# Kernel optimization log

Measured on AMD Instinct MI355X. Metric: run time of the kernel, lower is better.

Reference implementation:

```python
import jax, jax.numpy as jnp
import numpy as np

TEMPERATURE = 0.1
EPS = 1e-8


def setup_inputs() -> dict:
    key = jax.random.key(0)
    k1, k2 = jax.random.split(key)
    features = jax.random.normal(k1, (1024, 256, 16, 8), dtype=jnp.float32)
    labels = jax.random.randint(k2, (1024,), 0, 64, dtype=jnp.int64)
    return {"features": features, "labels": labels}


def reference(features, labels):
    B = features.shape[0]
    f = features.reshape(B, -1)
    norm = jnp.clip(jnp.linalg.norm(f, axis=1, keepdims=True), EPS)
    f = f / norm
    # matcher modeled as cosine-similarity gram matrix (opaque TransMatcher out of scope)
    scores = (f @ f.T) / TEMPERATURE  # [B, B]

    same = labels[:, None] == labels[None, :]
    eye = jnp.eye(B, dtype=bool)
    pos = same & ~eye  # positives excluding self
    neg = ~same & ~eye  # negatives excluding self

    # shared max over pos ∪ neg = all off-diagonal entries per row (matches original)
    row_max = jnp.max(jnp.where(eye, -jnp.inf, scores), axis=1, keepdims=True)
    e = jnp.exp(scores - row_max)  # [B, B]
    pos_sum = jnp.sum(jnp.where(pos, e, 0.0), axis=1)
    neg_sum = jnp.sum(jnp.where(neg, e, 0.0), axis=1)

    valid = jnp.any(pos, axis=1) & jnp.any(neg, axis=1)
    safe_pos = jnp.where(valid, pos_sum, 1.0)
    safe_neg = jnp.where(valid, neg_sum, 1.0)
    # loss_i = neg_term - pos_term; shared max cancels
    loss_i = jnp.where(valid, jnp.log(safe_neg) - jnp.log(safe_pos), 0.0)

    total = jnp.sum(valid.astype(jnp.float32))
    loss = jnp.where(total > 0, jnp.sum(loss_i) / jnp.maximum(total, 1.0), 0.0)

    max_pos = jnp.max(jnp.where(pos, scores, -jnp.inf), axis=1)
    max_neg = jnp.max(jnp.where(neg, scores, -jnp.inf), axis=1)
    correct = jnp.sum((valid & (max_pos > max_neg)).astype(jnp.float32))
    accuracy = jnp.where(total > 0, correct / jnp.maximum(total, 1.0), 0.5)
    return loss, accuracy
```

## Files before the change

kernel.cpp:

```cpp
#include <hip/hip_runtime.h>
#include <hip/hip_bf16.h>
#include <stdint.h>

#define BSZ 1024
#define KF 32768
#define SPLITK 32
#define KPER (KF / SPLITK)
#define BKB 128
#define TEMP_INV 10.0f

typedef float f32x4 __attribute__((ext_vector_type(4)));

__device__ __forceinline__ void async_copy16(const void* g, void* l) {
    __builtin_amdgcn_global_load_lds(
        (const __attribute__((address_space(1))) void*)g,
        (__attribute__((address_space(3))) void*)l, 16, 0, 0);
}

__device__ __forceinline__ unsigned short f2bf_bits(float x) {
    union { float f; uint32_t u; } t; t.f = x;
    uint32_t r = t.u + 0x7FFFu + ((t.u >> 16) & 1u);
    return (unsigned short)(r >> 16);
}
__device__ __forceinline__ float bf2f(unsigned short b) {
    union { uint32_t u; float f; } t; t.u = ((uint32_t)b) << 16; return t.f;
}

__device__ __forceinline__ float waveSum(float v) {
    for (int o = 32; o > 0; o >>= 1) v += __shfl_down(v, o);
    return v;
}
__device__ __forceinline__ float waveMax(float v) {
    for (int o = 32; o > 0; o >>= 1) v = fmaxf(v, __shfl_down(v, o));
    return v;
}
__device__ __forceinline__ float blockSum(float v, float* red, int tid) {
    v = waveSum(v);
    __syncthreads();
    if ((tid & 63) == 0) red[tid >> 6] = v;
    __syncthreads();
    return red[0] + red[1] + red[2] + red[3];
}
__device__ __forceinline__ float blockMax(float v, float* red, int tid) {
    v = waveMax(v);
    __syncthreads();
    if ((tid & 63) == 0) red[tid >> 6] = v;
    __syncthreads();
    return fmaxf(fmaxf(red[0], red[1]), fmaxf(red[2], red[3]));
}

__global__ __launch_bounds__(256) void k_norm_convert(
    const float* __restrict__ f, unsigned char* __restrict__ f8,
    float* __restrict__ inv_norm) {
    int row = blockIdx.x, tid = threadIdx.x;
    const float4* src = (const float4*)(f + (size_t)row * KF);
    int4* dst = (int4*)(f8 + (size_t)row * KF);
    float ss = 0.f;
    for (int o = 0; o < 8; ++o) {
        int base4 = o * 1024 + tid * 4;
        int4 pk;
        int* pkp = &pk.x;
#pragma unroll
        for (int q = 0; q < 4; ++q) {
            float4 v = src[base4 + q];
            ss += v.x * v.x + v.y * v.y + v.z * v.z + v.w * v.w;
            int wd = __builtin_amdgcn_cvt_pk_fp8_f32(v.x, v.y, 0, false);
            wd = __builtin_amdgcn_cvt_pk_fp8_f32(v.z, v.w, wd, true);
            pkp[q] = wd;
        }
        dst[o * 256 + tid] = pk;
    }
    __shared__ float red[4];
    float tot = blockSum(ss, red, tid);
    if (tid == 0) inv_norm[row] = 1.0f / fmaxf(sqrtf(tot), 1e-8f);
}

__global__ __launch_bounds__(256) void k_gemm(
    const unsigned char* __restrict__ f8, unsigned short* __restrict__ partials) {
    __shared__ unsigned char Alds[128 * BKB];
    __shared__ unsigned char Blds[128 * BKB];
    int tid = threadIdx.x;

    int t = blockIdx.x;
    int bi = 0, accu = 0;
    while (accu + bi + 1 <= t) { accu += bi + 1; ++bi; }
    int bj = t - accu;
    int row0 = bi * 128, col0 = bj * 128;
    int p = blockIdx.y;
    size_t kbase = (size_t)p * KPER;

    const unsigned char* Ag = f8 + (size_t)row0 * KF;
    const unsigned char* Bg = f8 + (size_t)col0 * KF;
    int lane = tid & 63, w = tid >> 6;
    int wrow = (w >> 1) * 64, wcol = (w & 1) * 64;
    int mrow = lane & 15, quad = lane >> 4;

    int r_st[4], g_st[4];
#pragma unroll
    for (int c = 0; c < 4; ++c) {
        int idx = c * 256 + tid;
        r_st[c] = idx >> 3;
        g_st[c] = (idx & 7) ^ (r_st[c] & 7);
    }

    f32x4 acc[4][4] = {};

    for (int kt = 0; kt < KPER / BKB; ++kt) {
        size_t k0 = kbase + (size_t)kt * BKB;
        __syncthreads();
#pragma unroll
        for (int c = 0; c < 4; ++c) {
            int idx = c * 256 + tid;
            async_copy16(Ag + (size_t)r_st[c] * KF + k0 + g_st[c] * 16, &Alds[idx * 16]);
            async_copy16(Bg + (size_t)r_st[c] * KF + k0 + g_st[c] * 16, &Blds[idx * 16]);
        }
        __syncthreads();
#pragma unroll
        for (int ks = 0; ks < 4; ++ks) {
            long av[4], bv[4];
            int chunk = ks * 2 + (quad >> 1);
            int sub = (quad & 1) * 8;
#pragma unroll
            for (int mi = 0; mi < 4; ++mi) {
                int row = wrow + mi * 16 + mrow;
                av[mi] = *(const long*)&Alds[row * BKB + (chunk ^ (row & 7)) * 16 + sub];
            }
#pragma unroll
            for (int ni = 0; ni < 4; ++ni) {
                int row = wcol + ni * 16 + mrow;
                bv[ni] = *(const long*)&Blds[row * BKB + (chunk ^ (row & 7)) * 16 + sub];
            }
#pragma unroll
            for (int mi = 0; mi < 4; ++mi)
#pragma unroll
                for (int ni = 0; ni < 4; ++ni)
                    acc[mi][ni] = __builtin_amdgcn_mfma_f32_16x16x32_fp8_fp8(
                        av[mi], bv[ni], acc[mi][ni], 0, 0, 0);
        }
    }

    unsigned short* outp = partials + (size_t)p * BSZ * BSZ;
#pragma unroll
    for (int mi = 0; mi < 4; ++mi)
#pragma unroll
        for (int ni = 0; ni < 4; ++ni)
#pragma unroll
            for (int r = 0; r < 4; ++r) {
                int row = row0 + wrow + mi * 16 + quad * 4 + r;
                int col = col0 + wcol + ni * 16 + mrow;
                outp[(size_t)row * BSZ + col] = f2bf_bits(acc[mi][ni][r]);
            }
    if (bi != bj) {
#pragma unroll
        for (int mi = 0; mi < 4; ++mi)
#pragma unroll
            for (int ni = 0; ni < 4; ++ni) {
                int rowm = col0 + wcol + ni * 16 + mrow;
                int colm = row0 + wrow + mi * 16 + quad * 4;
                ushort4 v;
                v.x = f2bf_bits(acc[mi][ni][0]);
                v.y = f2bf_bits(acc[mi][ni][1]);
                v.z = f2bf_bits(acc[mi][ni][2]);
                v.w = f2bf_bits(acc[mi][ni][3]);
                *(ushort4*)&outp[(size_t)rowm * BSZ + colm] = v;
            }
    }
}

__global__ __launch_bounds__(256) void k_loss_rows(
    const unsigned short* __restrict__ partials, const float* __restrict__ inv_norm,
    const int* __restrict__ labels, float* __restrict__ rloss,
    float* __restrict__ rvalid, float* __restrict__ rcorr) {
    int i = blockIdx.x, tid = threadIdx.x;
    __shared__ float srow[BSZ];
    __shared__ int slab[BSZ];
    __shared__ float red[4];
    for (int c = 0; c < 4; ++c) slab[c * 256 + tid] = labels[c * 256 + tid];
    float inv_i = inv_norm[i];

    int j4 = tid * 4;
    float sx = 0.f, sy = 0.f, sz = 0.f, sw = 0.f;
#pragma unroll
    for (int p2 = 0; p2 < SPLITK; ++p2) {
        ushort4 v = *(const ushort4*)&partials[(size_t)p2 * BSZ * BSZ + (size_t)i * BSZ + j4];
        sx += bf2f(v.x); sy += bf2f(v.y); sz += bf2f(v.z); sw += bf2f(v.w);
    }
    float4 invj = *(const float4*)&inv_norm[j4];
    srow[j4 + 0] = sx * inv_i * invj.x * TEMP_INV;
    srow[j4 + 1] = sy * inv_i * invj.y * TEMP_INV;
    srow[j4 + 2] = sz * inv_i * invj.z * TEMP_INV;
    srow[j4 + 3] = sw * inv_i * invj.w * TEMP_INV;
    __syncthreads();

    int lab_i = slab[i];
    float lm = -3.0e38f;
    for (int c = 0; c < 4; ++c) {
        int j = c * 256 + tid;
        if (j != i) lm = fmaxf(lm, srow[j]);
    }
    float rowmax = blockMax(lm, red, tid);

    float pos_sum = 0.f, neg_sum = 0.f, mp = -3.0e38f, mn = -3.0e38f;
    for (int c = 0; c < 4; ++c) {
        int j = c * 256 + tid;
        if (j == i) continue;
        float s = srow[j];
        float e = expf(s - rowmax);
        if (slab[j] == lab_i) { pos_sum += e; mp = fmaxf(mp, s); }
        else                  { neg_sum += e; mn = fmaxf(mn, s); }
    }
    float ps = blockSum(pos_sum, red, tid);
    float ns = blockSum(neg_sum, red, tid);
    float mpa = blockMax(mp, red, tid);
    float mna = blockMax(mn, red, tid);
    if (tid == 0) {
        bool valid = (mpa > -1.0e37f) && (mna > -1.0e37f);
        rloss[i]  = valid ? (logf(ns) - logf(ps)) : 0.f;
        rvalid[i] = valid ? 1.f : 0.f;
        rcorr[i]  = (valid && (mpa > mna)) ? 1.f : 0.f;
    }
}

__global__ __launch_bounds__(256) void k_final(
    const float* __restrict__ rloss, const float* __restrict__ rvalid,
    const float* __restrict__ rcorr, float* __restrict__ out) {
    __shared__ float red[4];
    int tid = threadIdx.x;
    float sl = 0.f, sv = 0.f, sc = 0.f;
    for (int c = 0; c < 4; ++c) {
        int j = c * 256 + tid;
        sl += rloss[j]; sv += rvalid[j]; sc += rcorr[j];
    }
    sl = blockSum(sl, red, tid);
    sv = blockSum(sv, red, tid);
    sc = blockSum(sc, red, tid);
    if (tid == 0) {
        out[0] = (sv > 0.f) ? sl / fmaxf(sv, 1.f) : 0.f;
        out[1] = (sv > 0.f) ? sc / fmaxf(sv, 1.f) : 0.5f;
    }
}

extern "C" void kernel_launch(void* const* d_in, const int* in_sizes, int n_in,
                              void* d_out, int out_size, void* d_ws, size_t ws_size,
                              hipStream_t stream) {
    const float* feats = (const float*)d_in[0];
    const int* labels = (const int*)d_in[1];
    float* out = (float*)d_out;
    char* ws = (char*)d_ws;

    unsigned char* f8        = (unsigned char*)ws;
    unsigned short* partials = (unsigned short*)(ws + (size_t)32 * 1024 * 1024);
    float* inv_norm          = (float*)(ws + (size_t)96 * 1024 * 1024);
    float* rloss             = inv_norm + BSZ;
    float* rvalid            = rloss + BSZ;
    float* rcorr             = rvalid + BSZ;

    k_norm_convert<<<BSZ, 256, 0, stream>>>(feats, f8, inv_norm);
    k_gemm<<<dim3(36, SPLITK), 256, 0, stream>>>(f8, partials);
    k_loss_rows<<<BSZ, 256, 0, stream>>>(partials, inv_norm, labels, rloss, rvalid, rcorr);
    k_final<<<1, 256, 0, stream>>>(rloss, rvalid, rcorr, out);
}
```

Before: 270.4 us.

## Use 16x16x128 scaled FP8 MFMA and load A operand directly from global

Replaces four 16x16x32 FP8 MFMAs per k-tile with a single 16x16x128 mfma_scale instruction using neutral scales (0x7F). A-operand tiles are loaded straight from global memory into registers instead of being staged through LDS, which halves the shared-memory footprint. Launch bounds now request 3 blocks per CU for occupancy. The direct global loads for A are not coalesced across the 128-row tile and are not prefetched, so they may add latency stalls.

```diff
diff --git a/kernel.cpp b/kernel.cpp
--- a/kernel.cpp
+++ b/kernel.cpp
@@ -10,6 +10,7 @@
 #define TEMP_INV 10.0f
 
 typedef float f32x4 __attribute__((ext_vector_type(4)));
+typedef int v8i __attribute__((ext_vector_type(8)));
 
 __device__ __forceinline__ void async_copy16(const void* g, void* l) {
     __builtin_amdgcn_global_load_lds(
@@ -75,9 +76,8 @@
     if (tid == 0) inv_norm[row] = 1.0f / fmaxf(sqrtf(tot), 1e-8f);
 }
 
-__global__ __launch_bounds__(256) void k_gemm(
+__global__ __launch_bounds__(256, 3) void k_gemm(
     const unsigned char* __restrict__ f8, unsigned short* __restrict__ partials) {
-    __shared__ unsigned char Alds[128 * BKB];
     __shared__ unsigned char Blds[128 * BKB];
     int tid = threadIdx.x;
 
@@ -103,40 +103,46 @@
         g_st[c] = (idx & 7) ^ (r_st[c] & 7);
     }
 
+    const int4* Arow[4];
+#pragma unroll
+    for (int mi = 0; mi < 4; ++mi)
+        Arow[mi] = (const int4*)(Ag + (size_t)(wrow + mi * 16 + mrow) * KF
+                                 + kbase + quad * 32);
+
     f32x4 acc[4][4] = {};
 
     for (int kt = 0; kt < KPER / BKB; ++kt) {
         size_t k0 = kbase + (size_t)kt * BKB;
         __syncthreads();
 #pragma unroll
-        for (int c = 0; c < 4; ++c) {
-            int idx = c * 256 + tid;
-            async_copy16(Ag + (size_t)r_st[c] * KF + k0 + g_st[c] * 16, &Alds[idx * 16]);
-            async_copy16(Bg + (size_t)r_st[c] * KF + k0 + g_st[c] * 16, &Blds[idx * 16]);
+        for (int c = 0; c < 4; ++c)
+            async_copy16(Bg + (size_t)r_st[c] * KF + k0 + g_st[c] * 16,
+                         &Blds[(c * 256 + tid) * 16]);
+        v8i a8[4];
+#pragma unroll
+        for (int mi = 0; mi < 4; ++mi) {
+            int4 lo = Arow[mi][kt * 8];
+            int4 hi = Arow[mi][kt * 8 + 1];
+            a8[mi] = (v8i){lo.x, lo.y, lo.z, lo.w, hi.x, hi.y, hi.z, hi.w};
         }
         __syncthreads();
-#pragma unroll
-        for (int ks = 0; ks < 4; ++ks) {
-            long av[4], bv[4];
-            int chunk = ks * 2 + (quad >> 1);
-            int sub = (quad & 1) * 8;
-#pragma unroll
-            for (int mi = 0; mi < 4; ++mi) {
-                int row = wrow + mi * 16 + mrow;
-                av[mi] = *(const long*)&Alds[row * BKB + (chunk ^ (row & 7)) * 16 + sub];
-            }
-#pragma unroll
-            for (int ni = 0; ni < 4; ++ni) {
-                int row = wcol + ni * 16 + mrow;
-                bv[ni] = *(const long*)&Blds[row * BKB + (chunk ^ (row & 7)) * 16 + sub];
-            }
-#pragma unroll
-            for (int mi = 0; mi < 4; ++mi)
-#pragma unroll
-                for (int ni = 0; ni < 4; ++ni)
-                    acc[mi][ni] = __builtin_amdgcn_mfma_f32_16x16x32_fp8_fp8(
-                        av[mi], bv[ni], acc[mi][ni], 0, 0, 0);
+        v8i b8[4];
+#pragma unroll
+        for (int ni = 0; ni < 4; ++ni) {
+            int rB = wcol + ni * 16 + mrow;
+            int4 lo = *(const int4*)&Blds[rB * BKB + ((quad * 2)     ^ (rB & 7)) * 16];
+            int4 hi = *(const int4*)&Blds[rB * BKB + ((quad * 2 + 1) ^ (rB & 7)) * 16];
+            b8[ni] = (v8i){lo.x, lo.y, lo.z, lo.w, hi.x, hi.y, hi.z, hi.w};
         }
+#pragma unroll
+        for (int mi = 0; mi < 4; ++mi)
+#pragma unroll
+            for (int ni = 0; ni < 4; ++ni)
+                acc[mi][ni] = __builtin_amdgcn_mfma_scale_f32_16x16x128_f8f6f4(
+                    a8[mi], b8[ni], acc[mi][ni],
+                    0, 0,
+                    0, 0x7F7F7F7F,
+                    0, 0x7F7F7F7F);
     }
 
     unsigned short* outp = partials + (size_t)p * BSZ * BSZ;
```

New measurement: 280.8 us. +3.9%, slower.

## Double-buffer B tiles, load A directly to registers, fuse final reduction

Applied to the files above, without the earlier changes.

The GEMM now loads A fragments straight from global memory into registers and stages only B through LDS. B is double-buffered with async global-to-LDS copies issued two iterations ahead, and explicit vmcnt waits plus raw barriers replace the two __syncthreads per k-step, so loads overlap with MFMA work. The A reads take 32 contiguous bytes per lane and the B reads use 16-byte LDS loads, which changes the k-ordering of fragments consistently for both operands. The final single-block kernel is removed: per-row results are accumulated with atomics and the last block, found by a ticket counter, writes the outputs. This adds the risk of hand-tuned waitcnt correctness and atomic ordering of the float sums.

```diff
diff --git a/kernel.cpp b/kernel.cpp
--- a/kernel.cpp
+++ b/kernel.cpp
@@ -7,6 +7,7 @@
 #define SPLITK 32
 #define KPER (KF / SPLITK)
 #define BKB 128
+#define NITER (KPER / BKB)
 #define TEMP_INV 10.0f
 
 typedef float f32x4 __attribute__((ext_vector_type(4)));
@@ -51,8 +52,9 @@
 
 __global__ __launch_bounds__(256) void k_norm_convert(
     const float* __restrict__ f, unsigned char* __restrict__ f8,
-    float* __restrict__ inv_norm) {
+    float* __restrict__ inv_norm, float* __restrict__ gaccum) {
     int row = blockIdx.x, tid = threadIdx.x;
+    if (row == 0 && tid < 4) gaccum[tid] = 0.f;
     const float4* src = (const float4*)(f + (size_t)row * KF);
     int4* dst = (int4*)(f8 + (size_t)row * KF);
     float ss = 0.f;
@@ -77,8 +79,7 @@
 
 __global__ __launch_bounds__(256) void k_gemm(
     const unsigned char* __restrict__ f8, unsigned short* __restrict__ partials) {
-    __shared__ unsigned char Alds[128 * BKB];
-    __shared__ unsigned char Blds[128 * BKB];
+    __shared__ unsigned char Blds[2][128 * BKB];
     int tid = threadIdx.x;
 
     int t = blockIdx.x;
@@ -102,41 +103,63 @@
         r_st[c] = idx >> 3;
         g_st[c] = (idx & 7) ^ (r_st[c] & 7);
     }
-
-    f32x4 acc[4][4] = {};
-
-    for (int kt = 0; kt < KPER / BKB; ++kt) {
-        size_t k0 = kbase + (size_t)kt * BKB;
-        __syncthreads();
+    auto stageB = [&](int buf, size_t koff) {
 #pragma unroll
         for (int c = 0; c < 4; ++c) {
             int idx = c * 256 + tid;
-            async_copy16(Ag + (size_t)r_st[c] * KF + k0 + g_st[c] * 16, &Alds[idx * 16]);
-            async_copy16(Bg + (size_t)r_st[c] * KF + k0 + g_st[c] * 16, &Blds[idx * 16]);
-        }
-        __syncthreads();
-#pragma unroll
-        for (int ks = 0; ks < 4; ++ks) {
-            long av[4], bv[4];
-            int chunk = ks * 2 + (quad >> 1);
-            int sub = (quad & 1) * 8;
-#pragma unroll
-            for (int mi = 0; mi < 4; ++mi) {
-                int row = wrow + mi * 16 + mrow;
-                av[mi] = *(const long*)&Alds[row * BKB + (chunk ^ (row & 7)) * 16 + sub];
-            }
-#pragma unroll
-            for (int ni = 0; ni < 4; ++ni) {
-                int row = wcol + ni * 16 + mrow;
-                bv[ni] = *(const long*)&Blds[row * BKB + (chunk ^ (row & 7)) * 16 + sub];
-            }
+            async_copy16(Bg + (size_t)r_st[c] * KF + koff + g_st[c] * 16,
+                         &Blds[buf][idx * 16]);
+        }
+    };
+
+    const unsigned char* Aptr[4];
+#pragma unroll
+    for (int mi = 0; mi < 4; ++mi)
+        Aptr[mi] = Ag + (size_t)(wrow + mi * 16 + mrow) * KF + kbase + quad * 32;
+
+    f32x4 acc[4][4] = {};
+    union I4L2 { int4 v; long l[2]; };
+
+    stageB(0, kbase);
+    stageB(1, kbase + BKB);
+
+#pragma unroll
+    for (int kt = 0; kt < NITER; ++kt) {
+        int cur = kt & 1;
+        long a_l[4][4];
+#pragma unroll
+        for (int mi = 0; mi < 4; ++mi) {
+            I4L2 u0, u1;
+            u0.v = *(const int4*)(Aptr[mi] + (size_t)kt * BKB);
+            u1.v = *(const int4*)(Aptr[mi] + (size_t)kt * BKB + 16);
+            a_l[mi][0] = u0.l[0]; a_l[mi][1] = u0.l[1];
+            a_l[mi][2] = u1.l[0]; a_l[mi][3] = u1.l[1];
+        }
+        if (kt < NITER - 1) asm volatile("s_waitcnt vmcnt(12)" ::: "memory");
+        else                asm volatile("s_waitcnt vmcnt(8)"  ::: "memory");
+        asm volatile("s_barrier" ::: "memory");
+
+        long b_l[4][4];
+#pragma unroll
+        for (int ni = 0; ni < 4; ++ni) {
+            int rB = wcol + ni * 16 + mrow;
+            I4L2 lo, hi;
+            lo.v = *(const int4*)&Blds[cur][rB * BKB + ((quad * 2)     ^ (rB & 7)) * 16];
+            hi.v = *(const int4*)&Blds[cur][rB * BKB + ((quad * 2 + 1) ^ (rB & 7)) * 16];
+            b_l[ni][0] = lo.l[0]; b_l[ni][1] = lo.l[1];
+            b_l[ni][2] = hi.l[0]; b_l[ni][3] = hi.l[1];
+        }
+#pragma unroll
+        for (int ts = 0; ts < 4; ++ts)
 #pragma unroll
             for (int mi = 0; mi < 4; ++mi)
 #pragma unroll
                 for (int ni = 0; ni < 4; ++ni)
                     acc[mi][ni] = __builtin_amdgcn_mfma_f32_16x16x32_fp8_fp8(
-                        av[mi], bv[ni], acc[mi][ni], 0, 0, 0);
-        }
+                        a_l[mi][ts], b_l[ni][ts], acc[mi][ni], 0, 0, 0);
+
+        asm volatile("s_barrier" ::: "memory");
+        if (kt + 2 < NITER) stageB(cur, kbase + (size_t)(kt + 2) * BKB);
     }
 
     unsigned short* outp = partials + (size_t)p * BSZ * BSZ;
@@ -169,12 +192,13 @@
 
 __global__ __launch_bounds__(256) void k_loss_rows(
     const unsigned short* __restrict__ partials, const float* __restrict__ inv_norm,
-    const int* __restrict__ labels, float* __restrict__ rloss,
-    float* __restrict__ rvalid, float* __restrict__ rcorr) {
+    const int* __restrict__ labels, float* __restrict__ gaccum,
+    float* __restrict__ out) {
     int i = blockIdx.x, tid = threadIdx.x;
     __shared__ float srow[BSZ];
     __shared__ int slab[BSZ];
     __shared__ float red[4];
+    __shared__ int s_ticket;
     for (int c = 0; c < 4; ++c) slab[c * 256 + tid] = labels[c * 256 + tid];
     float inv_i = inv_norm[i];
 
@@ -213,28 +237,21 @@
     float ns = blockSum(neg_sum, red, tid);
     float mpa = blockMax(mp, red, tid);
     float mna = blockMax(mn, red, tid);
+
     if (tid == 0) {
         bool valid = (mpa > -1.0e37f) && (mna > -1.0e37f);
-        rloss[i]  = valid ? (logf(ns) - logf(ps)) : 0.f;
-        rvalid[i] = valid ? 1.f : 0.f;
-        rcorr[i]  = (valid && (mpa > mna)) ? 1.f : 0.f;
-    }
-}
-
-__global__ __launch_bounds__(256) void k_final(
-    const float* __restrict__ rloss, const float* __restrict__ rvalid,
-    const float* __restrict__ rcorr, float* __restrict__ out) {
-    __shared__ float red[4];
-    int tid = threadIdx.x;
-    float sl = 0.f, sv = 0.f, sc = 0.f;
-    for (int c = 0; c < 4; ++c) {
-        int j = c * 256 + tid;
-        sl += rloss[j]; sv += rvalid[j]; sc += rcorr[j];
-    }
-    sl = blockSum(sl, red, tid);
-    sv = blockSum(sv, red, tid);
-    sc = blockSum(sc, red, tid);
-    if (tid == 0) {
+        float li = valid ? (logf(ns) - logf(ps)) : 0.f;
+        atomicAdd(&gaccum[0], li);
+        atomicAdd(&gaccum[1], valid ? 1.f : 0.f);
+        atomicAdd(&gaccum[2], (valid && (mpa > mna)) ? 1.f : 0.f);
+        __threadfence();
+        s_ticket = atomicAdd((int*)&gaccum[3], 1);
+    }
+    __syncthreads();
+    if (s_ticket == BSZ - 1 && tid == 0) {
+        float sl = atomicAdd(&gaccum[0], 0.f);
+        float sv = atomicAdd(&gaccum[1], 0.f);
+        float sc = atomicAdd(&gaccum[2], 0.f);
         out[0] = (sv > 0.f) ? sl / fmaxf(sv, 1.f) : 0.f;
         out[1] = (sv > 0.f) ? sc / fmaxf(sv, 1.f) : 0.5f;
     }
@@ -251,12 +268,9 @@
     unsigned char* f8        = (unsigned char*)ws;
     unsigned short* partials = (unsigned short*)(ws + (size_t)32 * 1024 * 1024);
     float* inv_norm          = (float*)(ws + (size_t)96 * 1024 * 1024);
-    float* rloss             = inv_norm + BSZ;
-    float* rvalid            = rloss + BSZ;
-    float* rcorr             = rvalid + BSZ;
-
-    k_norm_convert<<<BSZ, 256, 0, stream>>>(feats, f8, inv_norm);
+    float* gaccum            = inv_norm + BSZ;
+
+    k_norm_convert<<<BSZ, 256, 0, stream>>>(feats, f8, inv_norm, gaccum);
     k_gemm<<<dim3(36, SPLITK), 256, 0, stream>>>(f8, partials);
-    k_loss_rows<<<BSZ, 256, 0, stream>>>(partials, inv_norm, labels, rloss, rvalid, rcorr);
-    k_final<<<1, 256, 0, stream>>>(rloss, rvalid, rcorr, out);
-}
+    k_loss_rows<<<BSZ, 256, 0, stream>>>(partials, inv_norm, labels, gaccum, out);
+}
```

New measurement: 323.4 us. +19.6%, slower.
